# Kernel tuning notes

Hardware: AMD Instinct MI355X
Metric: run time of the kernel (lower is better)

Reference implementation:

```python
import jax, jax.numpy as jnp
import numpy as np

NEG_BIG = -2.0**32 + 1.0

def setup_inputs() -> dict:
    key = jax.random.key(0)
    ks = jax.random.split(key, 8)
    B, T, D = 4096, 200, 32
    H1, H2 = 80, 40
    s = lambda n: 1.0 / np.sqrt(n)
    return {
        "q": jax.random.normal(ks[0], (B, D), jnp.float32),
        "k": jax.random.normal(ks[1], (B, T, D), jnp.float32),
        "v": jax.random.normal(ks[2], (B, T, D), jnp.float32),
        "mask": jax.random.randint(ks[3], (B, T), 0, 2, jnp.int32),
        "Wq": jax.random.normal(ks[4], (D, D), jnp.float32) * s(D),
        "bq": jnp.zeros((D,), jnp.float32),
        "alpha": jnp.zeros((D,), jnp.float32),  # Keras PReLU default alpha=0
        "W1": jax.random.normal(ks[5], (4 * D, H1), jnp.float32) * s(4 * D),
        "b1": jnp.zeros((H1,), jnp.float32),
        "W2": jax.random.normal(ks[6], (H1, H2), jnp.float32) * s(H1),
        "b2": jnp.zeros((H2,), jnp.float32),
        "Wf": jax.random.normal(ks[7], (H2, 1), jnp.float32) * s(H2),
        "bf": jnp.zeros((1,), jnp.float32),
    }

def prelu(x, a):
    return jnp.where(x >= 0, x, a * x)

def reference(q, k, v, mask, Wq, bq, alpha, W1, b1, W2, b2, Wf, bf):
    # dense_q with PReLU activation: [B, D] -> [B, 32]
    qp = prelu(q @ Wq + bq, alpha)
    # tile query across history steps: [B, T, 32]
    qt = jnp.broadcast_to(qp[:, None, :], k.shape)
    # DIN attention features: [B, T, 4*32]
    info = jnp.concatenate([qt, k, qt - k, qt * k], axis=-1)
    info = jax.nn.sigmoid(info @ W1 + b1)
    info = jax.nn.sigmoid(info @ W2 + b2)
    logits = (info @ Wf + bf).squeeze(-1)  # [B, T]
    logits = jnp.where(mask == 0, jnp.full_like(logits, NEG_BIG), logits)
    att = jax.nn.softmax(logits, axis=-1)
    return att[:, None, :]  # [B, 1, T]
```

## Files before the change

### kernel.cpp

```cpp
#include <hip/hip_runtime.h>
#include <math.h>

typedef float f32x4 __attribute__((ext_vector_type(4)));
typedef _Float16 f16;
typedef f16 f16x8 __attribute__((ext_vector_type(8)));
typedef unsigned int u32;
typedef u32 u32x2 __attribute__((ext_vector_type(2)));

#define BB 4096
#define TT 200
#define DD 32
#define H1 80
#define H2 40
#define SLAB_W 104

__device__ __align__(16) float g_BCj[DD * H1];
__device__ __align__(16) float g_Dj [DD * H1];
__device__ __align__(16) float g_ACj[DD * H1];
__device__ __align__(16) f16 g_w2h[9 * 64 * 8];

__device__ __forceinline__ float fast_sigmoid(float x) {
    return __builtin_amdgcn_rcpf(1.f + __expf(-x));
}

__global__ void pack_kernel(const float* __restrict__ W1, const float* __restrict__ W2) {
    int idx = blockIdx.x * 256 + threadIdx.x;
    if (idx < DD * H1) {
        int kk = idx / H1, j = idx % H1;
        g_BCj[idx] = W1[(32 + kk) * H1 + j] - W1[(64 + kk) * H1 + j];
        g_Dj [idx] = W1[(96 + kk) * H1 + j];
        g_ACj[idx] = W1[kk * H1 + j] + W1[(64 + kk) * H1 + j];
        return;
    }
    idx -= DD * H1;
    if (idx < 9 * 64 * 8) {
        int e = idx & 7, l = (idx >> 3) & 63, g = idx >> 9;
        int kt = g / 3, n = g % 3;
        int j   = kt * 32 + (l >> 4) * 8 + e;
        int col = n * 16 + (l & 15);
        float v = (j < H1 && col < H2) ? W2[j * H2 + col] : 0.f;
        g_w2h[idx] = (f16)v;
    }
}

__global__ __launch_bounds__(256) void din_mfma(
    const float* __restrict__ q, const float* __restrict__ k, const int* __restrict__ mask,
    const float* __restrict__ Wq, const float* __restrict__ bq, const float* __restrict__ alpha,
    const float* __restrict__ b1, const float* __restrict__ b2, const float* __restrict__ Wf,
    float* __restrict__ out)
{
    const int tid = threadIdx.x;
    const int wid = tid >> 6, l = tid & 63;
    const int l15 = l & 15, lg4 = l >> 4;
    const int b   = (blockIdx.x << 2) | wid;

    __shared__ __align__(16) f16   slab[4][16][SLAB_W];
    __shared__ __align__(16) float u_s[4][H1];
    __shared__ __align__(16) float lgt[4][208];
    float* qp = lgt[wid];

    f16x8 W2r[9];
    #pragma unroll
    for (int g = 0; g < 9; ++g) W2r[g] = *(const f16x8*)(g_w2h + (g * 64 + l) * 8);

    const int* mrow = mask + (size_t)b * TT;
    int mk0 = mrow[l];
    int mk1 = mrow[64 + l];
    int mk2 = mrow[128 + l];
    int mk3 = (l < 8) ? mrow[192 + l] : 1;

    if (l < DD) {
        const float* qr = q + (size_t)b * DD;
        float acc = bq[l];
        #pragma unroll
        for (int e = 0; e < DD; ++e) acc += qr[e] * Wq[e * DD + l];
        float a = alpha[l];
        qp[l] = acc >= 0.f ? acc : a * acc;
    }
    {
        u32* z0 = (u32*)slab[wid];
        #pragma unroll
        for (int i = 0; i < 2; ++i) {
            int idx = i * 64 + l;
            z0[(idx >> 3) * 52 + 40 + (idx & 7)] = 0u;
        }
    }

    #pragma unroll
    for (int i = 0; i < 2; ++i) {
        int c = i * 64 + l;
        if (c < H1) {
            float acc = b1[c];
            #pragma unroll
            for (int d = 0; d < DD; ++d) acc += qp[d] * g_ACj[d * H1 + c];
            u_s[wid][c] = acc;
        }
    }
    f16x8 Bh[5];
    #pragma unroll
    for (int n = 0; n < 5; ++n) {
        #pragma unroll
        for (int e = 0; e < 8; ++e) {
            int kidx = lg4 * 8 + e;
            int j = n * 16 + l15;
            Bh[n][e] = (f16)(g_BCj[kidx * H1 + j] + qp[kidx] * g_Dj[kidx * H1 + j]);
        }
    }
    f32x4 b2r[3], wfr[3];
    #pragma unroll
    for (int n = 0; n < 3; ++n) {
        int c0 = n * 16 + lg4 * 4;
        if (c0 + 3 < H2) {
            b2r[n] = *(const f32x4*)(b2 + c0);
            wfr[n] = *(const f32x4*)(Wf + c0);
        } else {
            b2r[n] = (f32x4){0.f, 0.f, 0.f, 0.f};
            wfr[n] = (f32x4){0.f, 0.f, 0.f, 0.f};
        }
    }
    f32x4 ur[5];
    #pragma unroll
    for (int n = 0; n < 5; ++n) ur[n] = *(const f32x4*)(&u_s[wid][n * 16 + lg4 * 4]);

    const float* kb = k + (size_t)b * (TT * DD);
    f16 (*ws)[SLAB_W] = slab[wid];
    float* lg = lgt[wid];

    f32x4 x0, x1;
    auto loadk = [&](int m) {
        int t = m * 16 + l15; if (t > TT - 1) t = TT - 1;
        const f32x4* kr = (const f32x4*)(kb + t * DD + lg4 * 8);
        x0 = kr[0]; x1 = kr[1];
    };

    auto l1_full = [&](int nload) {
        f16x8 Ah;
        #pragma unroll
        for (int e = 0; e < 4; ++e) {
            Ah[e]     = (f16)x0[e];
            Ah[e + 4] = (f16)x1[e];
        }
        if (nload >= 0) loadk(nload);
        #pragma unroll
        for (int n = 0; n < 5; ++n) {
            int j0 = n * 16 + lg4 * 4;
            f32x4 acc = ur[n];
            acc = __builtin_amdgcn_mfma_f32_16x16x32_f16(Bh[n], Ah, acc, 0, 0, 0);
            auto p01 = __builtin_amdgcn_cvt_pkrtz(fast_sigmoid(acc[0]), fast_sigmoid(acc[1]));
            auto p23 = __builtin_amdgcn_cvt_pkrtz(fast_sigmoid(acc[2]), fast_sigmoid(acc[3]));
            u32x2 w;
            w[0] = __builtin_bit_cast(u32, p01);
            w[1] = __builtin_bit_cast(u32, p23);
            *(u32x2*)(&ws[l15][j0]) = w;
        }
    };

    auto body = [&](int m) {
        f16x8 sh0 = *(const f16x8*)(&ws[l15][0 * 32 + lg4 * 8]);
        f16x8 sh1 = *(const f16x8*)(&ws[l15][1 * 32 + lg4 * 8]);
        f16x8 sh2 = *(const f16x8*)(&ws[l15][2 * 32 + lg4 * 8]);

        if (m < 12) l1_full(m < 11 ? m + 2 : -1);

        f32x4 a0 = {0.f,0.f,0.f,0.f}, a1 = {0.f,0.f,0.f,0.f}, a2 = {0.f,0.f,0.f,0.f};
        #pragma unroll
        for (int kt = 0; kt < 3; ++kt) {
            f16x8 sh = (kt == 0) ? sh0 : (kt == 1) ? sh1 : sh2;
            a0 = __builtin_amdgcn_mfma_f32_16x16x32_f16(W2r[kt * 3 + 0], sh, a0, 0, 0, 0);
            a1 = __builtin_amdgcn_mfma_f32_16x16x32_f16(W2r[kt * 3 + 1], sh, a1, 0, 0, 0);
            a2 = __builtin_amdgcn_mfma_f32_16x16x32_f16(W2r[kt * 3 + 2], sh, a2, 0, 0, 0);
        }

        float p = 0.f;
        #pragma unroll
        for (int n = 0; n < 3; ++n) {
            f32x4 av = (n == 0) ? a0 : (n == 1) ? a1 : a2;
            p += wfr[n][0] * fast_sigmoid(av[0] + b2r[n][0]);
            p += wfr[n][1] * fast_sigmoid(av[1] + b2r[n][1]);
            p += wfr[n][2] * fast_sigmoid(av[2] + b2r[n][2]);
            p += wfr[n][3] * fast_sigmoid(av[3] + b2r[n][3]);
        }
        p += __shfl_xor(p, 16);
        p += __shfl_xor(p, 32);
        if (l < 16) lg[m * 16 + l15] = p;
    };

    loadk(0);
    l1_full(1);

    for (int m = 0; m < 13; ++m) body(m);

    const float NEG = -4294967295.0f;
    float v0 = lg[l];        if (mk0 == 0) v0 = NEG;
    float v1 = lg[64 + l];   if (mk1 == 0) v1 = NEG;
    float v2 = lg[128 + l];  if (mk2 == 0) v2 = NEG;
    float v3 = -8589934590.0f;
    if (l < 8) { v3 = lg[192 + l]; if (mk3 == 0) v3 = NEG; }

    float mx = fmaxf(fmaxf(v0, v1), fmaxf(v2, v3));
    #pragma unroll
    for (int off = 32; off; off >>= 1) mx = fmaxf(mx, __shfl_xor(mx, off));

    float e0 = __expf(v0 - mx), e1 = __expf(v1 - mx);
    float e2 = __expf(v2 - mx), e3 = __expf(v3 - mx);
    float s = (e0 + e1) + (e2 + e3);
    #pragma unroll
    for (int off = 32; off; off >>= 1) s += __shfl_xor(s, off);

    float* orow = out + (size_t)b * TT;
    orow[l]       = e0 / s;
    orow[64 + l]  = e1 / s;
    orow[128 + l] = e2 / s;
    if (l < 8) orow[192 + l] = e3 / s;
}

extern "C" void kernel_launch(void* const* d_in, const int* in_sizes, int n_in,
                              void* d_out, int out_size, void* d_ws, size_t ws_size,
                              hipStream_t stream) {
    const float* q     = (const float*)d_in[0];
    const float* k     = (const float*)d_in[1];
    const int*   mask  = (const int*)d_in[3];
    const float* Wq    = (const float*)d_in[4];
    const float* bq    = (const float*)d_in[5];
    const float* alpha = (const float*)d_in[6];
    const float* W1    = (const float*)d_in[7];
    const float* b1    = (const float*)d_in[8];
    const float* W2    = (const float*)d_in[9];
    const float* b2    = (const float*)d_in[10];
    const float* Wf    = (const float*)d_in[11];
    float* out = (float*)d_out;

    hipLaunchKernelGGL(pack_kernel, dim3((DD * H1 + 9 * 64 * 8 + 255) / 256), dim3(256),
                       0, stream, W1, W2);
    hipLaunchKernelGGL(din_mfma, dim3(BB / 4), dim3(256), 0, stream,
                       q, k, mask, Wq, bq, alpha, b1, b2, Wf, out);
}
```

Baseline: 48.65 us.

## Split each batch row across two waves and fold log2e into weights

Result: slower. 58.60 us (+20.5%).

```diff
diff --git a/kernel.cpp b/kernel.cpp
--- a/kernel.cpp
+++ b/kernel.cpp
@@ -13,23 +13,29 @@
 #define H1 80
 #define H2 40
 #define SLAB_W 104
+#define LOG2E 1.44269504f
 
 __device__ __align__(16) float g_BCj[DD * H1];
 __device__ __align__(16) float g_Dj [DD * H1];
 __device__ __align__(16) float g_ACj[DD * H1];
 __device__ __align__(16) f16 g_w2h[9 * 64 * 8];
 
-__device__ __forceinline__ float fast_sigmoid(float x) {
-    return __builtin_amdgcn_rcpf(1.f + __expf(-x));
+__device__ __forceinline__ float exp2_raw(float x) {
+    float r;
+    asm("v_exp_f32 %0, %1" : "=v"(r) : "v"(x));
+    return r;
+}
+__device__ __forceinline__ float sig_pre(float a) {
+    return __builtin_amdgcn_rcpf(1.f + exp2_raw(a));
 }
 
 __global__ void pack_kernel(const float* __restrict__ W1, const float* __restrict__ W2) {
     int idx = blockIdx.x * 256 + threadIdx.x;
     if (idx < DD * H1) {
         int kk = idx / H1, j = idx % H1;
-        g_BCj[idx] = W1[(32 + kk) * H1 + j] - W1[(64 + kk) * H1 + j];
-        g_Dj [idx] = W1[(96 + kk) * H1 + j];
-        g_ACj[idx] = W1[kk * H1 + j] + W1[(64 + kk) * H1 + j];
+        g_BCj[idx] = -LOG2E * (W1[(32 + kk) * H1 + j] - W1[(64 + kk) * H1 + j]);
+        g_Dj [idx] = -LOG2E * W1[(96 + kk) * H1 + j];
+        g_ACj[idx] = -LOG2E * (W1[kk * H1 + j] + W1[(64 + kk) * H1 + j]);
         return;
     }
     idx -= DD * H1;
@@ -39,7 +45,7 @@
         int j   = kt * 32 + (l >> 4) * 8 + e;
         int col = n * 16 + (l & 15);
         float v = (j < H1 && col < H2) ? W2[j * H2 + col] : 0.f;
-        g_w2h[idx] = (f16)v;
+        g_w2h[idx] = (f16)(-LOG2E * v);
     }
 }
 
@@ -52,12 +58,13 @@
     const int tid = threadIdx.x;
     const int wid = tid >> 6, l = tid & 63;
     const int l15 = l & 15, lg4 = l >> 4;
-    const int b   = (blockIdx.x << 2) | wid;
+    const int r   = wid >> 1, s = wid & 1;
+    const int b   = (blockIdx.x << 1) | r;
 
     __shared__ __align__(16) f16   slab[4][16][SLAB_W];
-    __shared__ __align__(16) float u_s[4][H1];
-    __shared__ __align__(16) float lgt[4][208];
-    float* qp = lgt[wid];
+    __shared__ __align__(16) float qp_s[2][DD];
+    __shared__ __align__(16) float u_s[2][H1];
+    __shared__ __align__(16) float lgt[2][208];
 
     f16x8 W2r[9];
     #pragma unroll
@@ -69,13 +76,13 @@
     int mk2 = mrow[128 + l];
     int mk3 = (l < 8) ? mrow[192 + l] : 1;
 
-    if (l < DD) {
+    if (s == 0 && l < DD) {
         const float* qr = q + (size_t)b * DD;
         float acc = bq[l];
         #pragma unroll
         for (int e = 0; e < DD; ++e) acc += qr[e] * Wq[e * DD + l];
         float a = alpha[l];
-        qp[l] = acc >= 0.f ? acc : a * acc;
+        qp_s[r][l] = acc >= 0.f ? acc : a * acc;
     }
     {
         u32* z0 = (u32*)slab[wid];
@@ -86,14 +93,17 @@
         }
     }
 
+    __syncthreads();
+    const float* qp = qp_s[r];
+
     #pragma unroll
     for (int i = 0; i < 2; ++i) {
         int c = i * 64 + l;
         if (c < H1) {
-            float acc = b1[c];
+            float acc = -LOG2E * b1[c];
             #pragma unroll
             for (int d = 0; d < DD; ++d) acc += qp[d] * g_ACj[d * H1 + c];
-            u_s[wid][c] = acc;
+            u_s[r][c] = acc;
         }
     }
     f16x8 Bh[5];
@@ -111,8 +121,12 @@
     for (int n = 0; n < 3; ++n) {
         int c0 = n * 16 + lg4 * 4;
         if (c0 + 3 < H2) {
-            b2r[n] = *(const f32x4*)(b2 + c0);
-            wfr[n] = *(const f32x4*)(Wf + c0);
+            f32x4 bv = *(const f32x4*)(b2 + c0);
+            f32x4 wv = *(const f32x4*)(Wf + c0);
+            #pragma unroll
+            for (int e = 0; e < 4; ++e) { bv[e] *= -LOG2E; wv[e] *= LOG2E; }
+            b2r[n] = bv;
+            wfr[n] = wv;
         } else {
             b2r[n] = (f32x4){0.f, 0.f, 0.f, 0.f};
             wfr[n] = (f32x4){0.f, 0.f, 0.f, 0.f};
@@ -120,11 +134,11 @@
     }
     f32x4 ur[5];
     #pragma unroll
-    for (int n = 0; n < 5; ++n) ur[n] = *(const f32x4*)(&u_s[wid][n * 16 + lg4 * 4]);
+    for (int n = 0; n < 5; ++n) ur[n] = *(const f32x4*)(&u_s[r][n * 16 + lg4 * 4]);
 
     const float* kb = k + (size_t)b * (TT * DD);
     f16 (*ws)[SLAB_W] = slab[wid];
-    float* lg = lgt[wid];
+    float* lg = lgt[r];
 
     f32x4 x0, x1;
     auto loadk = [&](int m) {
@@ -146,8 +160,8 @@
             int j0 = n * 16 + lg4 * 4;
             f32x4 acc = ur[n];
             acc = __builtin_amdgcn_mfma_f32_16x16x32_f16(Bh[n], Ah, acc, 0, 0, 0);
-            auto p01 = __builtin_amdgcn_cvt_pkrtz(fast_sigmoid(acc[0]), fast_sigmoid(acc[1]));
-            auto p23 = __builtin_amdgcn_cvt_pkrtz(fast_sigmoid(acc[2]), fast_sigmoid(acc[3]));
+            auto p01 = __builtin_amdgcn_cvt_pkrtz(sig_pre(acc[0]), sig_pre(acc[1]));
+            auto p23 = __builtin_amdgcn_cvt_pkrtz(sig_pre(acc[2]), sig_pre(acc[3]));
             u32x2 w;
             w[0] = __builtin_bit_cast(u32, p01);
             w[1] = __builtin_bit_cast(u32, p23);
@@ -160,7 +174,7 @@
         f16x8 sh1 = *(const f16x8*)(&ws[l15][1 * 32 + lg4 * 8]);
         f16x8 sh2 = *(const f16x8*)(&ws[l15][2 * 32 + lg4 * 8]);
 
-        if (m < 12) l1_full(m < 11 ? m + 2 : -1);
+        if (m + 2 < 13) l1_full(m + 4 < 13 ? m + 4 : -1);
 
         f32x4 a0 = {0.f,0.f,0.f,0.f}, a1 = {0.f,0.f,0.f,0.f}, a2 = {0.f,0.f,0.f,0.f};
         #pragma unroll
@@ -171,24 +185,27 @@
             a2 = __builtin_amdgcn_mfma_f32_16x16x32_f16(W2r[kt * 3 + 2], sh, a2, 0, 0, 0);
         }
 
-        float p = 0.f;
+        float pn[3];
         #pragma unroll
         for (int n = 0; n < 3; ++n) {
             f32x4 av = (n == 0) ? a0 : (n == 1) ? a1 : a2;
-            p += wfr[n][0] * fast_sigmoid(av[0] + b2r[n][0]);
-            p += wfr[n][1] * fast_sigmoid(av[1] + b2r[n][1]);
-            p += wfr[n][2] * fast_sigmoid(av[2] + b2r[n][2]);
-            p += wfr[n][3] * fast_sigmoid(av[3] + b2r[n][3]);
-        }
+            float t0 = wfr[n][0] * sig_pre(av[0] + b2r[n][0]);
+            float t1 = wfr[n][1] * sig_pre(av[1] + b2r[n][1]);
+            float t2 = wfr[n][2] * sig_pre(av[2] + b2r[n][2]);
+            float t3 = wfr[n][3] * sig_pre(av[3] + b2r[n][3]);
+            pn[n] = (t0 + t1) + (t2 + t3);
+        }
+        float p = (pn[0] + pn[1]) + pn[2];
         p += __shfl_xor(p, 16);
         p += __shfl_xor(p, 32);
         if (l < 16) lg[m * 16 + l15] = p;
     };
 
-    loadk(0);
-    l1_full(1);
-
-    for (int m = 0; m < 13; ++m) body(m);
+    loadk(s);
+    l1_full(s + 2 < 13 ? s + 2 : -1);
+    for (int m = s; m < 13; m += 2) body(m);
+
+    __syncthreads();
 
     const float NEG = -4294967295.0f;
     float v0 = lg[l];        if (mk0 == 0) v0 = NEG;
@@ -201,17 +218,20 @@
     #pragma unroll
     for (int off = 32; off; off >>= 1) mx = fmaxf(mx, __shfl_xor(mx, off));
 
-    float e0 = __expf(v0 - mx), e1 = __expf(v1 - mx);
-    float e2 = __expf(v2 - mx), e3 = __expf(v3 - mx);
-    float s = (e0 + e1) + (e2 + e3);
-    #pragma unroll
-    for (int off = 32; off; off >>= 1) s += __shfl_xor(s, off);
+    float e0 = exp2_raw(v0 - mx), e1 = exp2_raw(v1 - mx);
+    float e2 = exp2_raw(v2 - mx), e3 = exp2_raw(v3 - mx);
+    float ssum = (e0 + e1) + (e2 + e3);
+    #pragma unroll
+    for (int off = 32; off; off >>= 1) ssum += __shfl_xor(ssum, off);
 
     float* orow = out + (size_t)b * TT;
-    orow[l]       = e0 / s;
-    orow[64 + l]  = e1 / s;
-    orow[128 + l] = e2 / s;
-    if (l < 8) orow[192 + l] = e3 / s;
+    if (s == 0) {
+        orow[l]      = e0 / ssum;
+        orow[64 + l] = e1 / ssum;
+    } else {
+        orow[128 + l] = e2 / ssum;
+        if (l < 8) orow[192 + l] = e3 / ssum;
+    }
 }
 
 extern "C" void kernel_launch(void* const* d_in, const int* in_sizes, int n_in,
@@ -232,6 +252,6 @@
 
     hipLaunchKernelGGL(pack_kernel, dim3((DD * H1 + 9 * 64 * 8 + 255) / 256), dim3(256),
                        0, stream, W1, W2);
-    hipLaunchKernelGGL(din_mfma, dim3(BB / 4), dim3(256), 0, stream,
+    hipLaunchKernelGGL(din_mfma, dim3(BB / 2), dim3(256), 0, stream,
                        q, k, mask, Wq, bq, alpha, b1, b2, Wf, out);
 }
```
